# Kernel optimization log

Hardware: AMD Instinct MI355X
Metric: run time of the kernel (lower is better)

The kernel has to match this reference:

```python
import jax, jax.numpy as jnp
import numpy as np
import math

D_MODEL = 1024
N_HEAD = 16
HEAD_DIM = D_MODEL // N_HEAD
BATCH = 4
MAX_LEN = 1024


def _shift(BD):
    # BD: (b, h, L, 2L) -> (b, h, L, L), Transformer-XL relative shift
    b, h, L, _ = BD.shape
    zero_pad = jnp.zeros((b, h, L, 1), BD.dtype)
    BD = jnp.concatenate([BD, zero_pad], axis=-1)      # (b,h,L,2L+1)
    BD = BD.reshape(b, h, -1, L)[:, :, :-1]            # (b,h,2L,L)
    BD = BD.reshape(b, h, L, -1)                       # (b,h,L,2L)
    return BD[:, :, :, L:]                             # (b,h,L,L)


def setup_inputs() -> dict:
    key = jax.random.key(0)
    ks = jax.random.split(key, 10)
    s = 1.0 / math.sqrt(D_MODEL)
    return {
        "q": jax.random.normal(ks[0], (BATCH, MAX_LEN, D_MODEL), jnp.float32),
        "k": jax.random.normal(ks[1], (BATCH, MAX_LEN, D_MODEL), jnp.float32),
        "mask": jax.random.randint(ks[2], (BATCH, MAX_LEN), 0, 2, jnp.int32),
        "pos_embed": jax.random.normal(ks[3], (2 * MAX_LEN, HEAD_DIM), jnp.float32),
        "Wq": jax.random.normal(ks[4], (D_MODEL, D_MODEL), jnp.float32) * s,
        "Wkv": jax.random.normal(ks[5], (D_MODEL, 2 * D_MODEL), jnp.float32) * s,
        "Wr": jax.random.normal(ks[6], (HEAD_DIM, HEAD_DIM), jnp.float32) / math.sqrt(HEAD_DIM),
        "r_r_bias": jax.random.normal(ks[7], (N_HEAD, HEAD_DIM), jnp.float32) * 0.02,
        "r_w_bias": jax.random.normal(ks[8], (N_HEAD, HEAD_DIM), jnp.float32) * 0.02,
    }


def reference(q, k, mask, pos_embed, Wq, Wkv, Wr, r_r_bias, r_w_bias):
    B, L, D = q.shape
    H = r_r_bias.shape[0]
    hd = D // H
    scale = math.sqrt(hd)

    r = pos_embed @ Wr                                   # (2L, hd)
    qh = (q @ Wq).reshape(B, L, H, hd).transpose(0, 2, 1, 3)   # (B,H,L,hd)
    kv = k @ Wkv                                         # (B,L,2D)
    kk, vv = jnp.split(kv, 2, axis=-1)
    kh = kk.reshape(B, L, H, hd).transpose(0, 2, 1, 3)
    vh = vv.reshape(B, L, H, hd).transpose(0, 2, 1, 3)

    AC = jnp.einsum('bhqd,bhkd->bhqk', qh + r_r_bias[None, :, None, :], kh)
    BD = jnp.einsum('bhqd,ld->bhql', qh + r_w_bias[None, :, None, :], r)  # (B,H,L,2L)
    BD = _shift(BD)

    attn = (AC + BD) / scale
    attn = jnp.where(mask[:, None, None, :] == 0, -jnp.inf, attn)
    attn = jax.nn.softmax(attn, axis=-1)

    out = jnp.einsum('bhqk,bhkd->bhqd', attn, vh)        # (B,H,L,hd)
    return out.transpose(0, 2, 1, 3).reshape(B, L, D)
```

## Files before the change

### kernel.cpp

```cpp
#include <hip/hip_runtime.h>

typedef short bf16x8 __attribute__((ext_vector_type(8)));
typedef float f32x4 __attribute__((ext_vector_type(4)));
typedef unsigned short u16;
typedef unsigned short u16x4 __attribute__((ext_vector_type(4)));
typedef unsigned short u16x8 __attribute__((ext_vector_type(8)));

#define NB 4
#define LEN 1024
#define DM 1024
#define NH 16
#define HD 64

#define QSCALE 0.18033688011112043f

__device__ __forceinline__ u16 f2bf(float f) {
    union { float f; unsigned u; } v; v.f = f;
    return (u16)((v.u + 0x7fffu + ((v.u >> 16) & 1u)) >> 16);
}

__device__ __forceinline__ float exp2f_fast(float x) {
    float r; asm("v_exp_f32 %0, %1" : "=v"(r) : "v"(x)); return r;
}

__device__ __forceinline__ unsigned cvt_pk_bf16(float a, float b) {
    unsigned r; asm("v_cvt_pk_bf16_f32 %0, %1, %2" : "=v"(r) : "v"(a), "v"(b)); return r;
}

__device__ __forceinline__ f32x4 mfma16(bf16x8 a, bf16x8 b, f32x4 c) {
    return __builtin_amdgcn_mfma_f32_16x16x32_bf16(a, b, c, 0, 0, 0);
}

__device__ __forceinline__ void gload16(const void* g, void* l) {
    __builtin_amdgcn_global_load_lds(
        (const __attribute__((address_space(1))) unsigned int*)g,
        (__attribute__((address_space(3))) unsigned int*)l, 16, 0, 0);
}

__global__ void cast_all(const float* __restrict__ q, const float* __restrict__ k,
                         const int* __restrict__ msk,
                         u16* __restrict__ qbf, u16* __restrict__ kbf,
                         float* __restrict__ mb) {
    int idx = blockIdx.x * 256 + threadIdx.x;
    if (idx < 1048576) {
        float4 v = ((const float4*)q)[idx];
        u16x4 o;
        o[0] = f2bf(v.x); o[1] = f2bf(v.y); o[2] = f2bf(v.z); o[3] = f2bf(v.w);
        ((u16x4*)qbf)[idx] = o;
    } else if (idx < 2097152) {
        int i = idx - 1048576;
        float4 v = ((const float4*)k)[i];
        u16x4 o;
        o[0] = f2bf(v.x); o[1] = f2bf(v.y); o[2] = f2bf(v.z); o[3] = f2bf(v.w);
        ((u16x4*)kbf)[i] = o;
    } else {
        int i = idx - 2097152;
        if (i < NB * LEN) mb[i] = msk[i] ? 0.f : -3.0e38f;
    }
}

__global__ void transWT(const float* __restrict__ Wq, const float* __restrict__ Wkv,
                        u16* __restrict__ WqT, u16* __restrict__ WkvT) {
    __shared__ float tile[32][33];
    const bool isQ = blockIdx.x < 32;
    const float* W = isQ ? Wq : Wkv;
    u16* WT = isQ ? WqT : WkvT;
    const int N = isQ ? 1024 : 2048;
    const int n0 = (isQ ? blockIdx.x : blockIdx.x - 32) * 32;
    const int k0 = blockIdx.y * 32;
    int tx = threadIdx.x, ty = threadIdx.y;
    #pragma unroll
    for (int j = 0; j < 4; j++) {
        int r = ty + j * 8;
        tile[r][tx] = W[(size_t)(k0 + r) * N + n0 + tx];
    }
    __syncthreads();
    #pragma unroll
    for (int j = 0; j < 4; j++) {
        int r = ty + j * 8;
        WT[(size_t)(n0 + r) * 1024 + k0 + tx] = f2bf(tile[tx][r]);
    }
}

__global__ void r_proj(const float* __restrict__ pos, const float* __restrict__ Wr,
                       u16* __restrict__ rbf) {
    int idx = blockIdx.x * 256 + threadIdx.x;
    if (idx >= 2064 * 64) return;
    int row = idx >> 6, col = idx & 63;
    float s = 0.f;
    if (row < 2048) {
        #pragma unroll
        for (int kk = 0; kk < 64; kk++) s += pos[row * 64 + kk] * Wr[kk * 64 + col];
    }
    const int csw = (((col >> 3) ^ (row & 7)) << 3) | (col & 7);
    rbf[(row << 6) | csw] = f2bf(s);
}

__global__ __launch_bounds__(256) void gemm_all(
    const u16* __restrict__ qbf, const u16* __restrict__ kbf,
    const u16* __restrict__ WqT, const u16* __restrict__ WkvT,
    const float* __restrict__ rrb, const float* __restrict__ rwb,
    u16* __restrict__ A1, u16* __restrict__ A2,
    u16* __restrict__ khs, u16* __restrict__ vhsT)
{
    __shared__ u16 as[2][128][32];
    __shared__ u16 bs[2][128][32];

    const int bx = blockIdx.x;
    const bool isQ = bx < 8;
    const u16* Abf = isQ ? qbf : kbf;
    const u16* BT  = isQ ? WqT : WkvT;
    const int n0 = (isQ ? bx : bx - 8) * 128;
    const int m0 = blockIdx.y * 128;
    const int tid = threadIdx.x;
    const int w = tid >> 6, lane = tid & 63, g = lane >> 4, c = lane & 15;
    const int wm = w >> 1, wn = w & 1;
    const int srow = lane >> 2, sj = lane & 3;

    const f32x4 fzero = {0.f, 0.f, 0.f, 0.f};
    f32x4 acc[4][4];
    #pragma unroll
    for (int i = 0; i < 4; i++)
        #pragma unroll
        for (int j = 0; j < 4; j++) acc[i][j] = fzero;

    auto STAGE = [&](int buf, int ks) {
        const int k0 = ks * 32;
        #pragma unroll
        for (int i = 0; i < 2; i++) {
            const int rb = w * 32 + i * 16;
            const int rowA = rb + srow;
            gload16(Abf + (size_t)(m0 + rowA) * 1024 + k0 + ((sj ^ (rowA & 3)) << 3),
                    &as[buf][rb][0]);
            gload16(BT + (size_t)(n0 + rowA) * 1024 + k0 + ((sj ^ (rowA & 3)) << 3),
                    &bs[buf][rb][0]);
        }
    };

    STAGE(0, 0);
    __syncthreads();

    for (int ks = 0; ks < 32; ks++) {
        const int cur = ks & 1, nb = cur ^ 1;
        if (ks < 31) STAGE(nb, ks + 1);

        bf16x8 af[4], bfr[4];
        #pragma unroll
        for (int i = 0; i < 4; i++) {
            const int row = wm * 64 + i * 16 + c;
            af[i] = *(const bf16x8*)&as[cur][row][(g ^ (row & 3)) << 3];
        }
        #pragma unroll
        for (int j = 0; j < 4; j++) {
            const int row = wn * 64 + j * 16 + c;
            bfr[j] = *(const bf16x8*)&bs[cur][row][(g ^ (row & 3)) << 3];
        }
        #pragma unroll
        for (int i = 0; i < 4; i++)
            #pragma unroll
            for (int j = 0; j < 4; j++)
                acc[i][j] = mfma16(af[i], bfr[j], acc[i][j]);

        __syncthreads();
    }

    #pragma unroll
    for (int j = 0; j < 4; j++) {
        const int n = n0 + wn * 64 + j * 16 + c;
        float b1v = 0.f, b2v = 0.f;
        if (isQ) { b1v = rrb[n]; b2v = rwb[n]; }
        #pragma unroll
        for (int i = 0; i < 4; i++) {
            const int l0 = m0 + wm * 64 + i * 16 + 4 * g;
            if (!isQ && n >= DM) {
                const int d = n & 63, hh = (n - DM) >> 6;
                const int bb = l0 >> 10, l = l0 & 1023;
                u16x4 o;
                #pragma unroll
                for (int r = 0; r < 4; r++) o[r] = f2bf(acc[i][j][r]);
                *(u16x4*)(vhsT + (((size_t)(bb * NH + hh)) * HD + d) * LEN + l) = o;
            } else {
                #pragma unroll
                for (int r = 0; r < 4; r++) {
                    const int row = l0 + r;
                    const int bb = row >> 10, l = row & 1023;
                    const float v = acc[i][j][r];
                    if (isQ) {
                        size_t idx = (((size_t)(bb * NH + (n >> 6))) * LEN + l) * HD + (n & 63);
                        A1[idx] = f2bf((v + b1v) * QSCALE);
                        A2[idx] = f2bf((v + b2v) * QSCALE);
                    } else {
                        const int d = n & 63;
                        const int dsw = (((d >> 3) ^ (l & 7)) << 3) | (d & 7);
                        size_t idx = (((size_t)(bb * NH + (n >> 6))) * LEN + l) * HD + dsw;
                        khs[idx] = f2bf(v);
                    }
                }
            }
        }
    }
}

__global__ __launch_bounds__(256, 2) void attn_kernel(
    const u16* __restrict__ A1, const u16* __restrict__ A2,
    const u16* __restrict__ khs, const u16* __restrict__ vhsT,
    const u16* __restrict__ rbf, const float* __restrict__ mbias,
    float* __restrict__ outp)
{
    __shared__ u16 kbuf[2][32][64];
    __shared__ u16 rbuf[192][64];
    __shared__ u16 vbuf[2][4][64][8];
    __shared__ float biasl[1024];
    __shared__ float gl[4][2][16][52];
    __shared__ u16 pl[4][32][40];

    const int bh = blockIdx.x;
    const int b = bh >> 4, h = bh & 15;
    const int tid = threadIdx.x;
    const int w = tid >> 6, lane = tid & 63, g = lane >> 4, c = lane & 15;
    const int q0 = blockIdx.y * 128, q0w = q0 + w * 32;
    const int lrow8 = lane >> 3, lcol = lane & 7;
    const int kkey = (c + 1) & 7;

    const u16* Kbase = khs + (size_t)bh * LEN * HD;
    const u16* Vp = vhsT + (size_t)bh * HD * LEN;
    u16* plw = &pl[w][0][0];

    const u16* A1p = A1 + ((size_t)bh * LEN + q0w) * HD;
    const u16* A2p = A2 + ((size_t)bh * LEN + q0w) * HD;
    bf16x8 a1f[2][2], a2f[2][2];
    #pragma unroll
    for (int qs = 0; qs < 2; qs++)
        #pragma unroll
        for (int kf = 0; kf < 2; kf++) {
            a1f[qs][kf] = *(const bf16x8*)(A1p + (qs * 16 + c) * HD + kf * 32 + g * 8);
            a2f[qs][kf] = *(const bf16x8*)(A2p + (qs * 16 + c) * HD + kf * 32 + g * 8);
        }

    gload16(mbias + b * LEN + w * 256 + lane * 4, &biasl[w * 256]);
    gload16(Kbase + (((size_t)(w * 8 + lrow8)) << 6) + (lcol << 3), &kbuf[0][w * 8][0]);
    gload16(Vp + ((size_t)lane << 10) + w * 8, &vbuf[0][w][0][0]);
    const int js0 = LEN - q0 - 128;
    #pragma unroll
    for (int i = 0; i < 5; i++) {
        const int jg = js0 + (w + 4 * i) * 8;
        gload16(rbf + (((size_t)(jg + lrow8)) << 6) + (lcol << 3), &rbuf[jg % 192][0]);
    }
    __syncthreads();

    int psl = (js0 + 160) % 192;
    int bsl = (LEN - q0w - 31) % 192;

    const f32x4 fzero = {0.f, 0.f, 0.f, 0.f};
    f32x4 oacc[2][4];
    #pragma unroll
    for (int qs = 0; qs < 2; qs++)
        #pragma unroll
        for (int dt = 0; dt < 4; dt++) oacc[qs][dt] = fzero;
    float mrow[2] = {-3.0e38f, -3.0e38f}, lrow[2] = {0.f, 0.f};

    for (int kt = 0; kt < 32; kt++) {
        const int cur = kt & 1, nb = cur ^ 1;
        const int c0 = kt * 32;

        if (kt < 31) {
            const int c0n = c0 + 32;
            gload16(Kbase + (((size_t)(c0n + w * 8 + lrow8)) << 6) + (lcol << 3), &kbuf[nb][w * 8][0]);
            gload16(Vp + ((size_t)lane << 10) + c0n + w * 8, &vbuf[nb][w][0][0]);
            const int pg = js0 + 160 + 32 * kt + 8 * w;
            int ps = psl + 8 * w; if (ps >= 192) ps -= 192;
            gload16(rbf + (((size_t)(pg + lrow8)) << 6) + (lcol << 3), &rbuf[ps][0]);
        }

        bf16x8 Kf[2][2];
        #pragma unroll
        for (int ct = 0; ct < 2; ct++)
            #pragma unroll
            for (int kf = 0; kf < 2; kf++)
                Kf[ct][kf] = *(const bf16x8*)&kbuf[cur][16 * ct + c][((4 * kf + g) ^ (c & 7)) * 8];

        bf16x8 Rf[4][2];
        #pragma unroll
        for (int mt = 0; mt < 4; mt++) {
            int t = bsl + mt * 16 + c; if (t >= 192) t -= 192;
            #pragma unroll
            for (int kf = 0; kf < 2; kf++)
                Rf[mt][kf] = *(const bf16x8*)&rbuf[t][((4 * kf + g) ^ kkey) * 8];
        }

        f32x4 s[2][2];
        #pragma unroll
        for (int qs = 0; qs < 2; qs++)
            #pragma unroll
            for (int ct = 0; ct < 2; ct++) {
                f32x4 a = fzero;
                a = mfma16(Kf[ct][0], a1f[qs][0], a);
                a = mfma16(Kf[ct][1], a1f[qs][1], a);
                s[qs][ct] = a;
            }

        #pragma unroll
        for (int mt = 1; mt < 4; mt++) {
            f32x4 ga = fzero;
            ga = mfma16(Rf[mt][0], a2f[0][0], ga);
            ga = mfma16(Rf[mt][1], a2f[0][1], ga);
            *(f32x4*)&gl[w][0][c][(mt - 1) * 16 + 4 * g] = ga;
        }
        #pragma unroll
        for (int mt = 0; mt < 3; mt++) {
            f32x4 ga = fzero;
            ga = mfma16(Rf[mt][0], a2f[1][0], ga);
            ga = mfma16(Rf[mt][1], a2f[1][1], ga);
            *(f32x4*)&gl[w][1][c][mt * 16 + 4 * g] = ga;
        }

        const float* glq0 = &gl[w][0][c][0];
        const float* glq1 = &gl[w][1][c][0];
        f32x4 bb0 = *(const f32x4*)&biasl[c0 + 4 * g];
        f32x4 bb1 = *(const f32x4*)&biasl[c0 + 16 + 4 * g];
        #pragma unroll
        for (int r = 0; r < 4; r++) {
            const int gidx = 4 * g + r + 15 - c;
            s[0][0][r] += glq0[gidx] + bb0[r];
            s[0][1][r] += glq0[gidx + 16] + bb1[r];
            s[1][0][r] += glq1[gidx] + bb0[r];
            s[1][1][r] += glq1[gidx + 16] + bb1[r];
        }

        bf16x8 Vb[4];
        #pragma unroll
        for (int dt = 0; dt < 4; dt++)
            Vb[dt] = *(const bf16x8*)&vbuf[cur][g][16 * dt + c][0];

        #pragma unroll
        for (int qs = 0; qs < 2; qs++) {
            float t = fmaxf(fmaxf(fmaxf(s[qs][0][0], s[qs][0][1]), fmaxf(s[qs][0][2], s[qs][0][3])),
                            fmaxf(fmaxf(s[qs][1][0], s[qs][1][1]), fmaxf(s[qs][1][2], s[qs][1][3])));
            t = fmaxf(t, __shfl_xor(t, 16));
            t = fmaxf(t, __shfl_xor(t, 32));
            if (!__all(t <= mrow[qs] + 8.f)) {
                const float mnew = fmaxf(mrow[qs], t);
                const float alpha = exp2f_fast(mrow[qs] - mnew);
                mrow[qs] = mnew;
                lrow[qs] *= alpha;
                #pragma unroll
                for (int dt = 0; dt < 4; dt++)
                    #pragma unroll
                    for (int r = 0; r < 4; r++) oacc[qs][dt][r] *= alpha;
            }
            const float mref = mrow[qs];
            float p[8];
            float ps = 0.f;
            #pragma unroll
            for (int r = 0; r < 4; r++) {
                p[r] = exp2f_fast(s[qs][0][r] - mref);
                p[4 + r] = exp2f_fast(s[qs][1][r] - mref);
                ps += p[r] + p[4 + r];
            }
            lrow[qs] += ps;
            const unsigned d0 = cvt_pk_bf16(p[0], p[1]);
            const unsigned d1 = cvt_pk_bf16(p[2], p[3]);
            const unsigned d2 = cvt_pk_bf16(p[4], p[5]);
            const unsigned d3 = cvt_pk_bf16(p[6], p[7]);
            const int prow = (qs * 16 + c) * 40;
            *(uint2*)&plw[prow + 4 * g] = make_uint2(d0, d1);
            *(uint2*)&plw[prow + 16 + 4 * g] = make_uint2(d2, d3);
            bf16x8 pbr = *(const bf16x8*)&plw[prow + 8 * g];
            #pragma unroll
            for (int dt = 0; dt < 4; dt++)
                oacc[qs][dt] = mfma16(Vb[dt], pbr, oacc[qs][dt]);
        }

        psl += 32; if (psl >= 192) psl -= 192;
        bsl += 32; if (bsl >= 192) bsl -= 192;
        __syncthreads();
    }

    #pragma unroll
    for (int qs = 0; qs < 2; qs++) {
        float sum = lrow[qs];
        sum += __shfl_xor(sum, 16);
        sum += __shfl_xor(sum, 32);
        const float inv = sum > 0.f ? 1.0f / sum : 0.f;
        const int l = q0w + qs * 16 + c;
        float* op = outp + ((size_t)b * LEN + l) * DM + h * HD;
        #pragma unroll
        for (int dt = 0; dt < 4; dt++) {
            f32x4 o;
            #pragma unroll
            for (int r = 0; r < 4; r++) o[r] = oacc[qs][dt][r] * inv;
            *(f32x4*)(op + dt * 16 + 4 * g) = o;
        }
    }
}

extern "C" void kernel_launch(void* const* d_in, const int* in_sizes, int n_in,
                              void* d_out, int out_size, void* d_ws, size_t ws_size,
                              hipStream_t stream) {
    const float* q   = (const float*)d_in[0];
    const float* k   = (const float*)d_in[1];
    const int*   msk = (const int*)d_in[2];
    const float* pos = (const float*)d_in[3];
    const float* Wq  = (const float*)d_in[4];
    const float* Wkv = (const float*)d_in[5];
    const float* Wr  = (const float*)d_in[6];
    const float* rrb = (const float*)d_in[7];
    const float* rwb = (const float*)d_in[8];
    float* outp = (float*)d_out;
    char* ws = (char*)d_ws;

    u16* qbf  = (u16*)(ws + 0);
    u16* kbf  = (u16*)(ws + 8388608);
    u16* WqT  = (u16*)(ws + 16777216);
    u16* WkvT = (u16*)(ws + 18874368);
    u16* rbf  = (u16*)(ws + 23068672);
    u16* A1   = (u16*)(ws + 23332864);
    u16* A2   = (u16*)(ws + 31721472);
    u16* khs  = (u16*)(ws + 40110080);
    u16* vhsT = (u16*)(ws + 48498688);
    float* mb = (float*)(ws + 56887296);

    cast_all<<<8208, 256, 0, stream>>>(q, k, msk, qbf, kbf, mb);
    transWT<<<dim3(96, 32), dim3(32, 8), 0, stream>>>(Wq, Wkv, WqT, WkvT);
    r_proj<<<516, 256, 0, stream>>>(pos, Wr, rbf);
    gemm_all<<<dim3(24, 32), 256, 0, stream>>>(qbf, kbf, WqT, WkvT, rrb, rwb, A1, A2, khs, vhsT);
    attn_kernel<<<dim3(64, 8), 256, 0, stream>>>(A1, A2, khs, vhsT, rbf, mb, outp);
}
```

Before: 124.7 us.

## Fuse fp32-to-bf16 cast into GEMM and load K/V/bias directly to registers

Removes the separate cast kernel. The GEMM now reads fp32 q/k through registers, converts them to bf16 and writes them to LDS, overlapping this work with the MFMA loop. The mask-bias setup moves into the r_proj kernel. In the attention kernel, K, V and mask bias are no longer staged through LDS; they are double-buffered in registers, loaded straight from global memory one tile ahead, and the K swizzle is dropped. This cuts a kernel launch and a full HBM round trip for q/k, and frees LDS in the attention kernel. The cost is higher register pressure and fp32 global reads inside the GEMM loop, which may slow it down.

```diff
diff --git a/kernel.cpp b/kernel.cpp
--- a/kernel.cpp
+++ b/kernel.cpp
@@ -5,6 +5,8 @@
 typedef unsigned short u16;
 typedef unsigned short u16x4 __attribute__((ext_vector_type(4)));
 typedef unsigned short u16x8 __attribute__((ext_vector_type(8)));
+typedef unsigned int u32;
+typedef unsigned int u32x4 __attribute__((ext_vector_type(4)));
 
 #define NB 4
 #define LEN 1024
@@ -35,28 +37,6 @@
     __builtin_amdgcn_global_load_lds(
         (const __attribute__((address_space(1))) unsigned int*)g,
         (__attribute__((address_space(3))) unsigned int*)l, 16, 0, 0);
-}
-
-__global__ void cast_all(const float* __restrict__ q, const float* __restrict__ k,
-                         const int* __restrict__ msk,
-                         u16* __restrict__ qbf, u16* __restrict__ kbf,
-                         float* __restrict__ mb) {
-    int idx = blockIdx.x * 256 + threadIdx.x;
-    if (idx < 1048576) {
-        float4 v = ((const float4*)q)[idx];
-        u16x4 o;
-        o[0] = f2bf(v.x); o[1] = f2bf(v.y); o[2] = f2bf(v.z); o[3] = f2bf(v.w);
-        ((u16x4*)qbf)[idx] = o;
-    } else if (idx < 2097152) {
-        int i = idx - 1048576;
-        float4 v = ((const float4*)k)[i];
-        u16x4 o;
-        o[0] = f2bf(v.x); o[1] = f2bf(v.y); o[2] = f2bf(v.z); o[3] = f2bf(v.w);
-        ((u16x4*)kbf)[i] = o;
-    } else {
-        int i = idx - 2097152;
-        if (i < NB * LEN) mb[i] = msk[i] ? 0.f : -3.0e38f;
-    }
 }
 
 __global__ void transWT(const float* __restrict__ Wq, const float* __restrict__ Wkv,
@@ -83,21 +63,26 @@
 }
 
 __global__ void r_proj(const float* __restrict__ pos, const float* __restrict__ Wr,
-                       u16* __restrict__ rbf) {
+                       const int* __restrict__ msk,
+                       u16* __restrict__ rbf, float* __restrict__ mb) {
     int idx = blockIdx.x * 256 + threadIdx.x;
-    if (idx >= 2064 * 64) return;
-    int row = idx >> 6, col = idx & 63;
-    float s = 0.f;
-    if (row < 2048) {
-        #pragma unroll
-        for (int kk = 0; kk < 64; kk++) s += pos[row * 64 + kk] * Wr[kk * 64 + col];
-    }
-    const int csw = (((col >> 3) ^ (row & 7)) << 3) | (col & 7);
-    rbf[(row << 6) | csw] = f2bf(s);
+    if (idx < 2064 * 64) {
+        int row = idx >> 6, col = idx & 63;
+        float s = 0.f;
+        if (row < 2048) {
+            #pragma unroll
+            for (int kk = 0; kk < 64; kk++) s += pos[row * 64 + kk] * Wr[kk * 64 + col];
+        }
+        const int csw = (((col >> 3) ^ (row & 7)) << 3) | (col & 7);
+        rbf[(row << 6) | csw] = f2bf(s);
+    } else {
+        int i = idx - 132096;
+        if (i < NB * LEN) mb[i] = msk[i] ? 0.f : -3.0e38f;
+    }
 }
 
 __global__ __launch_bounds__(256) void gemm_all(
-    const u16* __restrict__ qbf, const u16* __restrict__ kbf,
+    const float* __restrict__ qf, const float* __restrict__ kf32,
     const u16* __restrict__ WqT, const u16* __restrict__ WkvT,
     const float* __restrict__ rrb, const float* __restrict__ rwb,
     u16* __restrict__ A1, u16* __restrict__ A2,
@@ -108,7 +93,7 @@
 
     const int bx = blockIdx.x;
     const bool isQ = bx < 8;
-    const u16* Abf = isQ ? qbf : kbf;
+    const float* Af = isQ ? qf : kf32;
     const u16* BT  = isQ ? WqT : WkvT;
     const int n0 = (isQ ? bx : bx - 8) * 128;
     const int m0 = blockIdx.y * 128;
@@ -116,6 +101,7 @@
     const int w = tid >> 6, lane = tid & 63, g = lane >> 4, c = lane & 15;
     const int wm = w >> 1, wn = w & 1;
     const int srow = lane >> 2, sj = lane & 3;
+    const int arow = tid >> 1, ahalf = tid & 1;
 
     const f32x4 fzero = {0.f, 0.f, 0.f, 0.f};
     f32x4 acc[4][4];
@@ -124,25 +110,40 @@
         #pragma unroll
         for (int j = 0; j < 4; j++) acc[i][j] = fzero;
 
-    auto STAGE = [&](int buf, int ks) {
+    float4 fa[4];
+    const float* Abase = Af + (size_t)(m0 + arow) * 1024 + ahalf * 16;
+
+    auto STAGE_LOAD = [&](int ks, int buf) {
         const int k0 = ks * 32;
+        const float4* Ap = (const float4*)(Abase + k0);
+        fa[0] = Ap[0]; fa[1] = Ap[1]; fa[2] = Ap[2]; fa[3] = Ap[3];
         #pragma unroll
         for (int i = 0; i < 2; i++) {
             const int rb = w * 32 + i * 16;
-            const int rowA = rb + srow;
-            gload16(Abf + (size_t)(m0 + rowA) * 1024 + k0 + ((sj ^ (rowA & 3)) << 3),
-                    &as[buf][rb][0]);
-            gload16(BT + (size_t)(n0 + rowA) * 1024 + k0 + ((sj ^ (rowA & 3)) << 3),
+            const int rowB = rb + srow;
+            gload16(BT + (size_t)(n0 + rowB) * 1024 + k0 + ((sj ^ (rowB & 3)) << 3),
                     &bs[buf][rb][0]);
         }
     };
 
-    STAGE(0, 0);
+    auto STAGE_WRITE = [&](int buf) {
+        u32x4 d0, d1;
+        d0[0] = cvt_pk_bf16(fa[0].x, fa[0].y); d0[1] = cvt_pk_bf16(fa[0].z, fa[0].w);
+        d0[2] = cvt_pk_bf16(fa[1].x, fa[1].y); d0[3] = cvt_pk_bf16(fa[1].z, fa[1].w);
+        d1[0] = cvt_pk_bf16(fa[2].x, fa[2].y); d1[1] = cvt_pk_bf16(fa[2].z, fa[2].w);
+        d1[2] = cvt_pk_bf16(fa[3].x, fa[3].y); d1[3] = cvt_pk_bf16(fa[3].z, fa[3].w);
+        const int j0 = 2 * ahalf, j1 = j0 + 1;
+        *(u32x4*)&as[buf][arow][((j0 ^ (arow & 3)) << 3)] = d0;
+        *(u32x4*)&as[buf][arow][((j1 ^ (arow & 3)) << 3)] = d1;
+    };
+
+    STAGE_LOAD(0, 0);
+    STAGE_WRITE(0);
     __syncthreads();
 
     for (int ks = 0; ks < 32; ks++) {
         const int cur = ks & 1, nb = cur ^ 1;
-        if (ks < 31) STAGE(nb, ks + 1);
+        if (ks < 31) STAGE_LOAD(ks + 1, nb);
 
         bf16x8 af[4], bfr[4];
         #pragma unroll
@@ -161,6 +162,7 @@
             for (int j = 0; j < 4; j++)
                 acc[i][j] = mfma16(af[i], bfr[j], acc[i][j]);
 
+        if (ks < 31) STAGE_WRITE(nb);
         __syncthreads();
     }
 
@@ -190,9 +192,7 @@
                         A1[idx] = f2bf((v + b1v) * QSCALE);
                         A2[idx] = f2bf((v + b2v) * QSCALE);
                     } else {
-                        const int d = n & 63;
-                        const int dsw = (((d >> 3) ^ (l & 7)) << 3) | (d & 7);
-                        size_t idx = (((size_t)(bb * NH + (n >> 6))) * LEN + l) * HD + dsw;
+                        size_t idx = (((size_t)(bb * NH + (n >> 6))) * LEN + l) * HD + (n & 63);
                         khs[idx] = f2bf(v);
                     }
                 }
@@ -207,10 +207,7 @@
     const u16* __restrict__ rbf, const float* __restrict__ mbias,
     float* __restrict__ outp)
 {
-    __shared__ u16 kbuf[2][32][64];
     __shared__ u16 rbuf[192][64];
-    __shared__ u16 vbuf[2][4][64][8];
-    __shared__ float biasl[1024];
     __shared__ float gl[4][2][16][52];
     __shared__ u16 pl[4][32][40];
 
@@ -224,6 +221,7 @@
 
     const u16* Kbase = khs + (size_t)bh * LEN * HD;
     const u16* Vp = vhsT + (size_t)bh * HD * LEN;
+    const float* bp = mbias + b * LEN;
     u16* plw = &pl[w][0][0];
 
     const u16* A1p = A1 + ((size_t)bh * LEN + q0w) * HD;
@@ -237,15 +235,31 @@
             a2f[qs][kf] = *(const bf16x8*)(A2p + (qs * 16 + c) * HD + kf * 32 + g * 8);
         }
 
-    gload16(mbias + b * LEN + w * 256 + lane * 4, &biasl[w * 256]);
-    gload16(Kbase + (((size_t)(w * 8 + lrow8)) << 6) + (lcol << 3), &kbuf[0][w * 8][0]);
-    gload16(Vp + ((size_t)lane << 10) + w * 8, &vbuf[0][w][0][0]);
+    int koff[2][2], voff[4];
+    #pragma unroll
+    for (int ct = 0; ct < 2; ct++)
+        #pragma unroll
+        for (int kf = 0; kf < 2; kf++) koff[ct][kf] = (16 * ct + c) * HD + kf * 32 + g * 8;
+    #pragma unroll
+    for (int dt = 0; dt < 4; dt++) voff[dt] = (dt * 16 + c) * LEN + g * 8;
+
     const int js0 = LEN - q0 - 128;
     #pragma unroll
     for (int i = 0; i < 5; i++) {
         const int jg = js0 + (w + 4 * i) * 8;
         gload16(rbf + (((size_t)(jg + lrow8)) << 6) + (lcol << 3), &rbuf[jg % 192][0]);
     }
+    bf16x8 KA[2][2], KB[2][2], VA[4], VB[4];
+    f32x4 BA0, BA1, BB0, BB1;
+    #pragma unroll
+    for (int ct = 0; ct < 2; ct++)
+        #pragma unroll
+        for (int kf = 0; kf < 2; kf++)
+            KA[ct][kf] = *(const bf16x8*)(Kbase + koff[ct][kf]);
+    #pragma unroll
+    for (int dt = 0; dt < 4; dt++) VA[dt] = *(const bf16x8*)(Vp + voff[dt]);
+    BA0 = *(const f32x4*)(bp + 4 * g);
+    BA1 = *(const f32x4*)(bp + 16 + 4 * g);
     __syncthreads();
 
     int psl = (js0 + 160) % 192;
@@ -259,25 +273,27 @@
         for (int dt = 0; dt < 4; dt++) oacc[qs][dt] = fzero;
     float mrow[2] = {-3.0e38f, -3.0e38f}, lrow[2] = {0.f, 0.f};
 
-    for (int kt = 0; kt < 32; kt++) {
-        const int cur = kt & 1, nb = cur ^ 1;
+    auto STEP = [&](int kt, bf16x8 (&Kc)[2][2], bf16x8 (&Vc)[4], f32x4& Bc0, f32x4& Bc1,
+                    bf16x8 (&Kn)[2][2], bf16x8 (&Vn)[4], f32x4& Bn0, f32x4& Bn1) {
         const int c0 = kt * 32;
 
         if (kt < 31) {
-            const int c0n = c0 + 32;
-            gload16(Kbase + (((size_t)(c0n + w * 8 + lrow8)) << 6) + (lcol << 3), &kbuf[nb][w * 8][0]);
-            gload16(Vp + ((size_t)lane << 10) + c0n + w * 8, &vbuf[nb][w][0][0]);
             const int pg = js0 + 160 + 32 * kt + 8 * w;
             int ps = psl + 8 * w; if (ps >= 192) ps -= 192;
             gload16(rbf + (((size_t)(pg + lrow8)) << 6) + (lcol << 3), &rbuf[ps][0]);
         }
-
-        bf16x8 Kf[2][2];
+        const int cn = (kt < 31) ? c0 + 32 : c0;
         #pragma unroll
         for (int ct = 0; ct < 2; ct++)
             #pragma unroll
             for (int kf = 0; kf < 2; kf++)
-                Kf[ct][kf] = *(const bf16x8*)&kbuf[cur][16 * ct + c][((4 * kf + g) ^ (c & 7)) * 8];
+                Kn[ct][kf] = *(const bf16x8*)(Kbase + (size_t)cn * HD + koff[ct][kf]);
+        #pragma unroll
+        for (int dt = 0; dt < 4; dt++)
+            Vn[dt] = *(const bf16x8*)(Vp + voff[dt] + cn);
+        Bn0 = *(const f32x4*)(bp + cn + 4 * g);
+        Bn1 = *(const f32x4*)(bp + cn + 16 + 4 * g);
+        __builtin_amdgcn_sched_barrier(0);
 
         bf16x8 Rf[4][2];
         #pragma unroll
@@ -294,8 +310,8 @@
             #pragma unroll
             for (int ct = 0; ct < 2; ct++) {
                 f32x4 a = fzero;
-                a = mfma16(Kf[ct][0], a1f[qs][0], a);
-                a = mfma16(Kf[ct][1], a1f[qs][1], a);
+                a = mfma16(Kc[ct][0], a1f[qs][0], a);
+                a = mfma16(Kc[ct][1], a1f[qs][1], a);
                 s[qs][ct] = a;
             }
 
@@ -316,21 +332,14 @@
 
         const float* glq0 = &gl[w][0][c][0];
         const float* glq1 = &gl[w][1][c][0];
-        f32x4 bb0 = *(const f32x4*)&biasl[c0 + 4 * g];
-        f32x4 bb1 = *(const f32x4*)&biasl[c0 + 16 + 4 * g];
         #pragma unroll
         for (int r = 0; r < 4; r++) {
             const int gidx = 4 * g + r + 15 - c;
-            s[0][0][r] += glq0[gidx] + bb0[r];
-            s[0][1][r] += glq0[gidx + 16] + bb1[r];
-            s[1][0][r] += glq1[gidx] + bb0[r];
-            s[1][1][r] += glq1[gidx + 16] + bb1[r];
-        }
-
-        bf16x8 Vb[4];
-        #pragma unroll
-        for (int dt = 0; dt < 4; dt++)
-            Vb[dt] = *(const bf16x8*)&vbuf[cur][g][16 * dt + c][0];
+            s[0][0][r] += glq0[gidx] + Bc0[r];
+            s[0][1][r] += glq0[gidx + 16] + Bc1[r];
+            s[1][0][r] += glq1[gidx] + Bc0[r];
+            s[1][1][r] += glq1[gidx + 16] + Bc1[r];
+        }
 
         #pragma unroll
         for (int qs = 0; qs < 2; qs++) {
@@ -368,12 +377,17 @@
             bf16x8 pbr = *(const bf16x8*)&plw[prow + 8 * g];
             #pragma unroll
             for (int dt = 0; dt < 4; dt++)
-                oacc[qs][dt] = mfma16(Vb[dt], pbr, oacc[qs][dt]);
+                oacc[qs][dt] = mfma16(Vc[dt], pbr, oacc[qs][dt]);
         }
 
         psl += 32; if (psl >= 192) psl -= 192;
         bsl += 32; if (bsl >= 192) bsl -= 192;
         __syncthreads();
+    };
+
+    for (int kt2 = 0; kt2 < 16; kt2++) {
+        STEP(2 * kt2,     KA, VA, BA0, BA1, KB, VB, BB0, BB1);
+        STEP(2 * kt2 + 1, KB, VB, BB0, BB1, KA, VA, BA0, BA1);
     }
 
     #pragma unroll
@@ -409,8 +423,6 @@
     float* outp = (float*)d_out;
     char* ws = (char*)d_ws;
 
-    u16* qbf  = (u16*)(ws + 0);
-    u16* kbf  = (u16*)(ws + 8388608);
     u16* WqT  = (u16*)(ws + 16777216);
     u16* WkvT = (u16*)(ws + 18874368);
     u16* rbf  = (u16*)(ws + 23068672);
@@ -420,9 +432,8 @@
     u16* vhsT = (u16*)(ws + 48498688);
     float* mb = (float*)(ws + 56887296);
 
-    cast_all<<<8208, 256, 0, stream>>>(q, k, msk, qbf, kbf, mb);
     transWT<<<dim3(96, 32), dim3(32, 8), 0, stream>>>(Wq, Wkv, WqT, WkvT);
-    r_proj<<<516, 256, 0, stream>>>(pos, Wr, rbf);
-    gemm_all<<<dim3(24, 32), 256, 0, stream>>>(qbf, kbf, WqT, WkvT, rrb, rwb, A1, A2, khs, vhsT);
+    r_proj<<<532, 256, 0, stream>>>(pos, Wr, msk, rbf, mb);
+    gemm_all<<<dim3(24, 32), 256, 0, stream>>>(q, k, WqT, WkvT, rrb, rwb, A1, A2, khs, vhsT);
     attn_kernel<<<dim3(64, 8), 256, 0, stream>>>(A1, A2, khs, vhsT, rbf, mb, outp);
 }
```

New measurement: 147.6 us. 1.18x slower.
